# Performance work log

Hardware: AMD Instinct MI355X
Metric: run time of the kernel (lower is better)

The kernel has to match this reference:

```python
import jax, jax.numpy as jnp
import numpy as np
from jax import lax

IMG_W, IMG_H = 800.0, 320.0
NPTS = 72
N_STRIPS = NPTS - 1
MAX_LANES = 4
NUM_PRIORS = 192
STAGES = 3
B = 512
LIOU_LEN = 15.0
CLS_W, XYT_W, IOU_W, SEG_W = 2.0, 0.2, 2.0, 1.0


def smooth_l1(x):
    ax = jnp.abs(x)
    return jnp.where(ax < 1.0, 0.5 * x * x, ax - 0.5)


def pairwise_line_iou(pred_xs, tgt_xs):
    # pred_xs [P,N] pixel xs, tgt_xs [L,N]; returns [P,L]
    px1, px2 = pred_xs - LIOU_LEN, pred_xs + LIOU_LEN
    tx1, tx2 = tgt_xs - LIOU_LEN, tgt_xs + LIOU_LEN
    ovr = jnp.minimum(px2[:, None, :], tx2[None]) - jnp.maximum(px1[:, None, :], tx1[None])
    union = jnp.maximum(px2[:, None, :], tx2[None]) - jnp.minimum(px1[:, None, :], tx1[None])
    invalid = (tgt_xs < 0) | (tgt_xs >= IMG_W)
    ovr = jnp.where(invalid[None], 0.0, ovr)
    union = jnp.where(invalid[None], 0.0, union)
    return ovr.sum(-1) / (union.sum(-1) + 1e-9)


def focal_sum(logits, target):
    # kornia-style softmax focal loss (alpha=0.25, gamma=2), summed
    p = jax.nn.softmax(logits, axis=1) + 1e-8
    focal = -0.25 * (1.0 - p) ** 2 * jnp.log(p)
    oh = jax.nn.one_hot(target, 2, dtype=logits.dtype)
    return (oh * focal).sum()


def per_sample(pred, tgt):
    # pred [P, 6+N], tgt [L, 6+N]
    L = tgt.shape[0]
    f32 = pred.dtype
    valid = tgt[:, 1] == 1.0
    num_t = valid.sum()
    has_t = num_t > 0

    t_xs = tgt[:, 6:]                          # [L,N] pixel xs (-1e5 = invalid)
    pred_xs_px = pred[:, 6:] * (IMG_W - 1.0)   # [P,N]
    iou_pair = pairwise_line_iou(pred_xs_px, t_xs)  # [P,L] (grad flows for loss)

    # ---------- assignment (stop-grad, mirrors CLRNet dynamic_assign) ----------
    pd = lax.stop_gradient(pred)
    pd_xs = pd[:, 6:] * (IMG_W - 1.0)
    inv_t = (t_xs < 0) | (t_xs >= IMG_W)
    t_len = (~inv_t).sum(1).astype(f32)
    dist = jnp.where(inv_t[None], 0.0, jnp.abs(t_xs[None] - pd_xs[:, None, :])).sum(-1)
    dist = dist / (t_len[None] + 1e-9)         # [P,L]

    def norm_score(x):
        m = jnp.max(jnp.where(valid[None], x, -jnp.inf))
        m = jnp.where(has_t, m, 1.0)
        return 1.0 - x / m + 1e-2

    dist_score = norm_score(dist)
    p_xy = jnp.stack([pd[:, 2] * (IMG_H - 1.0), pd[:, 3] * (IMG_W - 1.0)], 1)
    t_xy = jnp.stack([tgt[:, 2] * (IMG_H - 1.0), tgt[:, 3]], 1)
    sd = jnp.sqrt(((p_xy[:, None] - t_xy[None]) ** 2).sum(-1))
    s_score = norm_score(sd)
    th = jnp.abs(pd[:, 4, None] - tgt[None, :, 4]) * 180.0
    th_score = norm_score(th)
    sp = jax.nn.sigmoid(pd[:, :2])
    neg = -jnp.log(1.0 - sp + 1e-12) * 0.75 * sp ** 2
    pos = -jnp.log(sp + 1e-12) * 0.25 * (1.0 - sp) ** 2
    cls_cost = pos[:, 1] - neg[:, 1]           # all gt labels are 1
    cost = -(dist_score * s_score * th_score) ** 2 * 3.0 + cls_cost[:, None]
    cost = jnp.where(valid[None], cost, jnp.inf)

    # dynamic-k (SimOTA-style)
    iou_sg = jnp.where(valid[None], jnp.maximum(lax.stop_gradient(iou_pair), 0.0), 0.0)
    topk = lax.top_k(iou_sg.T, 4)[0]           # [L,4]
    dyn_k = jnp.maximum(topk.sum(1).astype(jnp.int32), 1)
    ranks = jnp.argsort(jnp.argsort(cost, axis=0), axis=0)
    M = (ranks < dyn_k[None]) & valid[None]
    multi = M.sum(1) > 1
    argmin_col = jnp.argmin(cost, axis=1)
    Mf = M.astype(f32)
    Mf = Mf.at[:, 0].set(jnp.where(multi, 0.0, Mf[:, 0]))
    oh_min = jax.nn.one_hot(argmin_col, L, dtype=f32)
    Mf = jnp.where(multi[:, None] & (oh_min > 0), 1.0, Mf)
    n_match = Mf.sum()

    # ---------- cls loss ----------
    cls_target = (Mf.sum(1) > 0).astype(jnp.int32)
    cls_term = focal_sum(pred[:, :2], cls_target) / jnp.where(has_t, num_t.astype(f32), 1.0)

    # ---------- reg yxtl (smooth L1) ----------
    scale = jnp.array([N_STRIPS, IMG_W - 1.0, 180.0, N_STRIPS], dtype=f32)
    pred_yxtl = pred[:, 2:6] * scale           # [P,4]
    tgt3 = jnp.stack([tgt[:, 2] * N_STRIPS, tgt[:, 3], tgt[:, 4] * 180.0], 1)  # [L,3]
    pred_starts = jnp.clip(jnp.round(lax.stop_gradient(pred[:, 2]) * N_STRIPS), 0, N_STRIPS)
    tgt_starts = jnp.round(tgt[:, 2] * N_STRIPS)
    tgt_len_pair = tgt[None, :, 5] - (pred_starts[:, None] - tgt_starts[None, :])  # [P,L]
    sl = smooth_l1(pred_yxtl[:, None, :3] - tgt3[None]).sum(-1) \
       + smooth_l1(pred_yxtl[:, 3][:, None] - tgt_len_pair)
    reg_term = (Mf * sl).sum() / jnp.maximum(n_match * 4.0, 1.0)
    iou_term = (Mf * (1.0 - iou_pair)).sum() / jnp.maximum(n_match, 1.0)
    zero = jnp.zeros((), f32)
    reg_term = jnp.where(has_t, reg_term, zero)
    iou_term = jnp.where(has_t, iou_term, zero)
    return cls_term, reg_term, iou_term


def setup_inputs() -> dict:
    key = jax.random.key(0)
    ks = jax.random.split(key, 8)
    D = 6 + NPTS
    cls = jax.random.normal(ks[0], (STAGES, B, NUM_PRIORS, 2), jnp.float32)
    rest = jax.random.uniform(ks[1], (STAGES, B, NUM_PRIORS, D - 2), dtype=jnp.float32)
    predictions = jnp.concatenate([cls, rest], -1)

    valid = jax.random.uniform(ks[2], (B, MAX_LANES)) < 0.8
    start = jax.random.randint(ks[3], (B, MAX_LANES), 0, 40)
    length = jax.random.randint(ks[4], (B, MAX_LANES), 10, NPTS)
    end = jnp.minimum(start + length, NPTS)
    idx = jnp.arange(NPTS)
    inside = (idx[None, None] >= start[..., None]) & (idx[None, None] < end[..., None]) & valid[..., None]
    xs = jax.random.uniform(ks[5], (B, MAX_LANES, NPTS), minval=0.0, maxval=IMG_W - 1.0)
    xs = jnp.where(inside, xs, -1e5)
    start_x = jnp.take_along_axis(xs, start[..., None], axis=-1)[..., 0]
    theta = jax.random.uniform(ks[6], (B, MAX_LANES), minval=0.3, maxval=0.9)
    vf = valid.astype(jnp.float32)
    neg = jnp.full((B, MAX_LANES), -1e5, jnp.float32)
    targets = jnp.full((B, MAX_LANES, D), -1e5, jnp.float32)
    targets = targets.at[..., 0].set(1.0 - vf)
    targets = targets.at[..., 1].set(vf)
    targets = targets.at[..., 2].set(jnp.where(valid, start.astype(jnp.float32) / N_STRIPS, neg))
    targets = targets.at[..., 3].set(jnp.where(valid, start_x, neg))
    targets = targets.at[..., 4].set(jnp.where(valid, theta, neg))
    targets = targets.at[..., 5].set(jnp.where(valid, (end - start).astype(jnp.float32), neg))
    targets = targets.at[..., 6:].set(xs)

    seg_loss = jax.random.uniform(ks[7], (), dtype=jnp.float32)
    return {"predictions": predictions, "targets": targets, "seg_loss": seg_loss}


def reference(predictions, targets, seg_loss):
    per_batch = jax.vmap(per_sample)
    cls_l = jnp.zeros((), predictions.dtype)
    reg_l = jnp.zeros((), predictions.dtype)
    iou_l = jnp.zeros((), predictions.dtype)
    for s in range(predictions.shape[0]):  # 3 refine stages (fixed)
        c, r, i = per_batch(predictions[s], targets)
        cls_l = cls_l + c.sum()
        reg_l = reg_l + r.sum()
        iou_l = iou_l + i.sum()
    denom = targets.shape[0] * predictions.shape[0]
    cls_l = cls_l / denom
    reg_l = reg_l / denom
    iou_l = iou_l / denom
    return cls_l * CLS_W + reg_l * XYT_W + iou_l * IOU_W + seg_loss * SEG_W
```

## Files before the change

kernel.cpp:

```cpp
#include <hip/hip_runtime.h>
#include <math.h>

constexpr int kNpts   = 72;
constexpr int kPriors = 192;
constexpr int kLanes  = 4;
constexpr int kBatch  = 512;
constexpr int kStages = 3;
constexpr int kD      = 6 + kNpts;
constexpr int kChunkRows = 64;
constexpr int kChunkF = kChunkRows * kD;
constexpr int kChunkV4 = kChunkF / 4;

typedef unsigned long long u64;

__device__ __forceinline__ float smoothL1(float x) {
  float ax = fabsf(x);
  return ax < 1.0f ? 0.5f * x * x : ax - 0.5f;
}

__device__ __forceinline__ unsigned ordF(float f) {
  unsigned b = __float_as_uint(f);
  return (b & 0x80000000u) ? ~b : (b | 0x80000000u);
}

__device__ __forceinline__ void cswapA(u64& a, u64& b) {
  if (b < a) { u64 t = a; a = b; b = t; }
}
__device__ __forceinline__ void cswapD(float& a, float& b) {
  if (b > a) { float t = a; a = b; b = t; }
}
__device__ __forceinline__ u64 umin64(u64 a, u64 b) { return a < b ? a : b; }
__device__ __forceinline__ u64 umax64(u64 a, u64 b) { return a < b ? b : a; }

__global__ void clr_init(const float* __restrict__ seg, float* __restrict__ out) {
  out[0] = seg[0];
}

__global__ __launch_bounds__(192) void clr_loss_kernel(
    const float* __restrict__ pred,
    const float* __restrict__ tgt,
    float* __restrict__ out) {
  const int blk  = blockIdx.x;
  const int b    = blk & (kBatch - 1);
  const int tid  = threadIdx.x;
  const int wav  = tid >> 6;
  const int lane = tid & 63;

  __shared__ alignas(16) float s_buf[2][kChunkF];
  __shared__ float s_tx[kNpts][kLanes];
  __shared__ float s_m [kNpts][kLanes];
  __shared__ float s_hdr[kLanes][6];
  __shared__ float s_cost[kLanes][kPriors];
  __shared__ float s_iou[kLanes][kPriors];
  __shared__ u64   s_k3[kLanes][3];
  __shared__ int   s_dk[kLanes];
  __shared__ float s_sc[3][4];

  const float*  gsrc = pred + (size_t)blk * (kPriors * kD);
  const float4* g4   = (const float4*)gsrc;

  const float* tg = tgt + (size_t)b * kLanes * kD;
  for (int t = tid; t < kLanes * kNpts; t += 192) {
    int j = t / kNpts, k = t - j * kNpts;
    float v = tg[j * kD + 6 + k];
    s_tx[k][j] = v;
    s_m [k][j] = (v >= 0.0f && v < 800.0f) ? 1.0f : 0.0f;
  }
  if (tid < kLanes * 6) {
    int j = tid / 6, c = tid - j * 6;
    s_hdr[j][c] = tg[j * kD + c];
  }
  if (tid < kLanes) {
    s_dk[tid] = 1; s_k3[tid][0] = 0; s_k3[tid][1] = 0; s_k3[tid][2] = 0;
  }

  {
    float4* d4 = (float4*)&s_buf[0][0];
#pragma unroll
    for (int it = 0; it < 6; ++it) d4[it * 192 + tid] = g4[it * 192 + tid];
    if (tid < kChunkV4 - 6 * 192) d4[1152 + tid] = g4[1152 + tid];
  }
  __syncthreads();

  bool validL[kLanes];
  int num_t = 0;
#pragma unroll
  for (int j = 0; j < kLanes; ++j) {
    validL[j] = (s_hdr[j][1] == 1.0f);
    num_t += validL[j] ? 1 : 0;
  }
  const bool has_t = num_t > 0;

  float p0 = 0, p1 = 0, p2v = 0, p3v = 0, p4v = 0, p5v = 0;
  float ds0 = 0, ds1 = 0, ds2 = 0, ds3 = 0;
  for (int p = 0; p < 3; ++p) {
    if (p < 2) {
      float4* d4 = (float4*)&s_buf[(p + 1) & 1][0];
      const float4* s4 = g4 + (p + 1) * kChunkV4;
#pragma unroll
      for (int it = 0; it < 6; ++it) d4[it * 192 + tid] = s4[it * 192 + tid];
      if (tid < kChunkV4 - 6 * 192) d4[1152 + tid] = s4[1152 + tid];
    }
    if (wav == p) {
      const float2* L2 = (const float2*)(&s_buf[p & 1][0] + lane * kD);
      float2 h0 = L2[0], h1 = L2[1], h2 = L2[2];
      p0 = h0.x; p1 = h0.y; p2v = h1.x; p3v = h1.y; p4v = h2.x; p5v = h2.y;
      const float4* tx4 = (const float4*)&s_tx[0][0];
      const float4* m4  = (const float4*)&s_m[0][0];
#pragma unroll
      for (int i = 0; i < 36; ++i) {
        float2 a = L2[3 + i];
        float pA = a.x * 799.0f, pB = a.y * 799.0f;
        float4 tA = tx4[2 * i],     mA = m4[2 * i];
        float4 tB = tx4[2 * i + 1], mB = m4[2 * i + 1];
        ds0 = fmaf(mA.x, fabsf(tA.x - pA), ds0);
        ds1 = fmaf(mA.y, fabsf(tA.y - pA), ds1);
        ds2 = fmaf(mA.z, fabsf(tA.z - pA), ds2);
        ds3 = fmaf(mA.w, fabsf(tA.w - pA), ds3);
        ds0 = fmaf(mB.x, fabsf(tB.x - pB), ds0);
        ds1 = fmaf(mB.y, fabsf(tB.y - pB), ds1);
        ds2 = fmaf(mB.z, fabsf(tB.z - pB), ds2);
        ds3 = fmaf(mB.w, fabsf(tB.w - pB), ds3);
      }
    }
    __syncthreads();
  }
  float dsA[kLanes] = {ds0, ds1, ds2, ds3};

  float iou[kLanes], dist[kLanes], sd[kLanes], th[kLanes];
  float md = -INFINITY, ms = -INFINITY, mt = -INFINITY;
  const float py = p2v * 319.0f, pxc = p3v * 799.0f;
#pragma unroll
  for (int j = 0; j < kLanes; ++j) {
    float tlen = validL[j] ? s_hdr[j][5] : 0.0f;
    float ovr = fmaf(tlen, 30.0f, -dsA[j]);
    float uni = fmaf(tlen, 30.0f,  dsA[j]) + 1e-9f;
    iou[j]  = ovr / uni;
    dist[j] = dsA[j] / (tlen + 1e-9f);
    float dy = py - s_hdr[j][2] * 319.0f;
    float dx = pxc - s_hdr[j][3];
    sd[j] = sqrtf(dy * dy + dx * dx);
    th[j] = fabsf(p4v - s_hdr[j][4]) * 180.0f;
    if (validL[j]) {
      md = fmaxf(md, dist[j]);
      ms = fmaxf(ms, sd[j]);
      mt = fmaxf(mt, th[j]);
    }
  }

#pragma unroll
  for (int off = 32; off; off >>= 1) {
    md = fmaxf(md, __shfl_down(md, off, 64));
    ms = fmaxf(ms, __shfl_down(ms, off, 64));
    mt = fmaxf(mt, __shfl_down(mt, off, 64));
  }
  if (lane == 0) { s_sc[wav][0] = md; s_sc[wav][1] = ms; s_sc[wav][2] = mt; }
  __syncthreads();
  md = fmaxf(fmaxf(s_sc[0][0], s_sc[1][0]), s_sc[2][0]);
  ms = fmaxf(fmaxf(s_sc[0][1], s_sc[1][1]), s_sc[2][1]);
  mt = fmaxf(fmaxf(s_sc[0][2], s_sc[1][2]), s_sc[2][2]);
  if (!has_t) { md = 1.0f; ms = 1.0f; mt = 1.0f; }

  const float sp1  = 1.0f / (1.0f + expf(-p1));
  const float neg1 = -logf(1.0f - sp1 + 1e-12f) * 0.75f * sp1 * sp1;
  const float om1  = 1.0f - sp1;
  const float pos1 = -logf(sp1 + 1e-12f) * 0.25f * om1 * om1;
  const float cls_cost = pos1 - neg1;

  float costr[kLanes];
#pragma unroll
  for (int j = 0; j < kLanes; ++j) {
    s_iou[j][tid] = validL[j] ? fmaxf(iou[j], 0.0f) : 0.0f;
    float c;
    if (validL[j]) {
      float a = (1.0f - dist[j] / md) + 0.01f;
      float s = (1.0f - sd[j] / ms) + 0.01f;
      float t = (1.0f - th[j] / mt) + 0.01f;
      float g = a * s * t;
      c = cls_cost - g * g * 3.0f;
    } else {
      c = INFINITY;
    }
    costr[j] = c;
    s_cost[j][tid] = c;
  }
  __syncthreads();

  for (int t = wav; t < 8; t += 3) {
    const int j = t & 3;
    if (!validL[j]) continue;
    if (t < 4) {
      float c0 = s_cost[j][lane], c1 = s_cost[j][lane + 64], c2 = s_cost[j][lane + 128];
      u64 k0 = ((u64)ordF(c0) << 32) | (unsigned)lane;
      u64 k1 = ((u64)ordF(c1) << 32) | (unsigned)(lane + 64);
      u64 k2 = ((u64)ordF(c2) << 32) | (unsigned)(lane + 128);
      cswapA(k0, k1); cswapA(k0, k2); cswapA(k1, k2);
#pragma unroll
      for (int off = 1; off < 64; off <<= 1) {
        u64 b0 = __shfl_xor(k0, off), b1 = __shfl_xor(k1, off), b2 = __shfl_xor(k2, off);
        u64 x0 = umin64(k0, b0), y0 = umax64(k0, b0);
        u64 x1 = umin64(k1, b1);
        u64 mc = umin64(k2, b2);
        k0 = x0;
        k2 = umin64(umax64(y0, x1), mc);
        k1 = umin64(y0, x1);
      }
      if (lane == 0) { s_k3[j][0] = k0; s_k3[j][1] = k1; s_k3[j][2] = k2; }
    } else {
      float t0 = s_iou[j][lane], t1 = s_iou[j][lane + 64], t2 = s_iou[j][lane + 128];
      float t3 = -1.0f;
      cswapD(t0, t1); cswapD(t0, t2); cswapD(t1, t2);
#pragma unroll
      for (int off = 1; off < 64; off <<= 1) {
        float b0 = __shfl_xor(t0, off), b1 = __shfl_xor(t1, off);
        float b2 = __shfl_xor(t2, off), b3 = __shfl_xor(t3, off);
        float m0 = fmaxf(t0, b3), m1 = fmaxf(t1, b2);
        float m2 = fmaxf(t2, b1), m3 = fmaxf(t3, b0);
        cswapD(m0, m2); cswapD(m1, m3); cswapD(m0, m1); cswapD(m2, m3);
        t0 = m0; t1 = m1; t2 = m2; t3 = m3;
      }
      if (lane == 0) {
        float s = ((t0 + t1) + t2) + t3;
        int dk = (int)s;
        if (dk < 1) dk = 1;
        if (dk > 3) dk = 3;
        s_dk[j] = dk;
      }
    }
  }
  __syncthreads();

  int Mi[kLanes];
  int msum = 0;
#pragma unroll
  for (int j = 0; j < kLanes; ++j) {
    u64 myk = ((u64)ordF(costr[j]) << 32) | (unsigned)tid;
    Mi[j] = (validL[j] && myk <= s_k3[j][s_dk[j] - 1]) ? 1 : 0;
    msum += Mi[j];
  }

  float amin = costr[0];
  int aidx = 0;
#pragma unroll
  for (int j = 1; j < kLanes; ++j)
    if (costr[j] < amin) { amin = costr[j]; aidx = j; }

  float Mf[kLanes];
#pragma unroll
  for (int j = 0; j < kLanes; ++j) Mf[j] = (float)Mi[j];
  if (msum > 1) {
    Mf[0] = 0.0f;
    Mf[aidx] = 1.0f;
  }

  const float mfsum = Mf[0] + Mf[1] + Mf[2] + Mf[3];
  const int cls_t = (mfsum > 0.0f) ? 1 : 0;

  const float mx = fmaxf(p0, p1);
  const float e0 = expf(p0 - mx), e1 = expf(p1 - mx);
  const float inv = 1.0f / (e0 + e1);
  const float q = (cls_t ? e1 : e0) * inv + 1e-8f;
  const float omq = 1.0f - q;
  const float focal = -0.25f * omq * omq * logf(q);

  const float pred_start = fminf(fmaxf(rintf(p2v * 71.0f), 0.0f), 71.0f);
  const float py0 = p2v * 71.0f, py1 = p3v * 799.0f, py2t = p4v * 180.0f, py3 = p5v * 71.0f;
  float regc = 0.0f, iouc = 0.0f;
#pragma unroll
  for (int j = 0; j < kLanes; ++j) {
    if (Mf[j] > 0.0f) {
      float t30 = s_hdr[j][2] * 71.0f;
      float t31 = s_hdr[j][3];
      float t32 = s_hdr[j][4] * 180.0f;
      float tstart = rintf(s_hdr[j][2] * 71.0f);
      float tlp = s_hdr[j][5] - (pred_start - tstart);
      regc += smoothL1(py0 - t30) + smoothL1(py1 - t31) + smoothL1(py2t - t32)
            + smoothL1(py3 - tlp);
      iouc += 1.0f - iou[j];
    }
  }

  float v0 = mfsum, v1 = focal, v2 = regc, v3 = iouc;
#pragma unroll
  for (int off = 32; off; off >>= 1) {
    v0 += __shfl_down(v0, off, 64);
    v1 += __shfl_down(v1, off, 64);
    v2 += __shfl_down(v2, off, 64);
    v3 += __shfl_down(v3, off, 64);
  }
  __syncthreads();
  if (lane == 0) {
    s_sc[wav][0] = v0; s_sc[wav][1] = v1; s_sc[wav][2] = v2; s_sc[wav][3] = v3;
  }
  __syncthreads();

  if (tid == 0) {
    float nm      = s_sc[0][0] + s_sc[1][0] + s_sc[2][0];
    float cls_sum = s_sc[0][1] + s_sc[1][1] + s_sc[2][1];
    float reg_sum = s_sc[0][2] + s_sc[1][2] + s_sc[2][2];
    float iou_sum = s_sc[0][3] + s_sc[1][3] + s_sc[2][3];

    float cls_term = cls_sum / (has_t ? (float)num_t : 1.0f);
    float reg_term = has_t ? reg_sum / fmaxf(nm * 4.0f, 1.0f) : 0.0f;
    float iou_term = has_t ? iou_sum / fmaxf(nm, 1.0f) : 0.0f;

    float sample = 2.0f * cls_term + 0.2f * reg_term + 2.0f * iou_term;
    atomicAdd(out, sample * (1.0f / (float)(kBatch * kStages)));
  }
}

extern "C" void kernel_launch(void* const* d_in, const int* in_sizes, int n_in,
                              void* d_out, int out_size, void* d_ws, size_t ws_size,
                              hipStream_t stream) {
  const float* pred = (const float*)d_in[0];
  const float* tgt  = (const float*)d_in[1];
  const float* seg  = (const float*)d_in[2];
  float* out = (float*)d_out;

  clr_init<<<1, 1, 0, stream>>>(seg, out);
  clr_loss_kernel<<<kStages * kBatch, 192, 0, stream>>>(pred, tgt, out);
}
```

Before: 165.5 us.

## Split each prior row across two threads and load rows directly into registers

```diff
diff --git a/kernel.cpp b/kernel.cpp
--- a/kernel.cpp
+++ b/kernel.cpp
@@ -7,9 +7,6 @@
 constexpr int kBatch  = 512;
 constexpr int kStages = 3;
 constexpr int kD      = 6 + kNpts;
-constexpr int kChunkRows = 64;
-constexpr int kChunkF = kChunkRows * kD;
-constexpr int kChunkV4 = kChunkF / 4;
 
 typedef unsigned long long u64;
 
@@ -36,7 +33,7 @@
   out[0] = seg[0];
 }
 
-__global__ __launch_bounds__(192) void clr_loss_kernel(
+__global__ __launch_bounds__(384) void clr_loss_kernel(
     const float* __restrict__ pred,
     const float* __restrict__ tgt,
     float* __restrict__ out) {
@@ -45,40 +42,44 @@
   const int tid  = threadIdx.x;
   const int wav  = tid >> 6;
   const int lane = tid & 63;
-
-  __shared__ alignas(16) float s_buf[2][kChunkF];
-  __shared__ float s_tx[kNpts][kLanes];
-  __shared__ float s_m [kNpts][kLanes];
-  __shared__ float s_hdr[kLanes][6];
-  __shared__ float s_cost[kLanes][kPriors];
-  __shared__ float s_iou[kLanes][kPriors];
-  __shared__ u64   s_k3[kLanes][3];
-  __shared__ int   s_dk[kLanes];
-  __shared__ float s_sc[3][4];
-
-  const float*  gsrc = pred + (size_t)blk * (kPriors * kD);
-  const float4* g4   = (const float4*)gsrc;
+  const bool prim = (wav < 3);
+  const int  pid  = prim ? tid : tid - 192;
+
+  __shared__ float  s_tx[kNpts][kLanes];
+  __shared__ float  s_m [kNpts][kLanes];
+  __shared__ float  s_hdr[kLanes][6];
+  __shared__ float4 s_part[kPriors];
+  __shared__ float  s_cost[kLanes][kPriors];
+  __shared__ float  s_iou[kLanes][kPriors];
+  __shared__ u64    s_k3[kLanes][3];
+  __shared__ int    s_dk[kLanes];
+  __shared__ float  s_sc[3][4];
 
   const float* tg = tgt + (size_t)b * kLanes * kD;
-  for (int t = tid; t < kLanes * kNpts; t += 192) {
-    int j = t / kNpts, k = t - j * kNpts;
+  if (tid < kLanes * kNpts) {
+    int j = tid / kNpts, k = tid - j * kNpts;
     float v = tg[j * kD + 6 + k];
     s_tx[k][j] = v;
     s_m [k][j] = (v >= 0.0f && v < 800.0f) ? 1.0f : 0.0f;
   }
-  if (tid < kLanes * 6) {
-    int j = tid / 6, c = tid - j * 6;
+  if (tid >= 384 - kLanes * 6) {
+    int t = tid - (384 - kLanes * 6);
+    int j = t / 6, c = t - j * 6;
     s_hdr[j][c] = tg[j * kD + c];
   }
-  if (tid < kLanes) {
-    s_dk[tid] = 1; s_k3[tid][0] = 0; s_k3[tid][1] = 0; s_k3[tid][2] = 0;
-  }
-
-  {
-    float4* d4 = (float4*)&s_buf[0][0];
-#pragma unroll
-    for (int it = 0; it < 6; ++it) d4[it * 192 + tid] = g4[it * 192 + tid];
-    if (tid < kChunkV4 - 6 * 192) d4[1152 + tid] = g4[1152 + tid];
+  if (tid >= 288 && tid < 288 + kLanes) {
+    int j = tid - 288;
+    s_dk[j] = 1; s_k3[j][0] = 0; s_k3[j][1] = 0; s_k3[j][2] = 0;
+  }
+
+  const float2* rowv = (const float2*)(pred + ((size_t)blk * kPriors + pid) * kD);
+  float2 r[20];
+  if (prim) {
+#pragma unroll
+    for (int i = 0; i < 20; ++i) r[i] = rowv[i];
+  } else {
+#pragma unroll
+    for (int i = 0; i < 19; ++i) r[i] = rowv[20 + i];
   }
   __syncthreads();
 
@@ -91,102 +92,111 @@
   }
   const bool has_t = num_t > 0;
 
+  float ds0 = 0, ds1 = 0, ds2 = 0, ds3 = 0;
   float p0 = 0, p1 = 0, p2v = 0, p3v = 0, p4v = 0, p5v = 0;
-  float ds0 = 0, ds1 = 0, ds2 = 0, ds3 = 0;
-  for (int p = 0; p < 3; ++p) {
-    if (p < 2) {
-      float4* d4 = (float4*)&s_buf[(p + 1) & 1][0];
-      const float4* s4 = g4 + (p + 1) * kChunkV4;
-#pragma unroll
-      for (int it = 0; it < 6; ++it) d4[it * 192 + tid] = s4[it * 192 + tid];
-      if (tid < kChunkV4 - 6 * 192) d4[1152 + tid] = s4[1152 + tid];
-    }
-    if (wav == p) {
-      const float2* L2 = (const float2*)(&s_buf[p & 1][0] + lane * kD);
-      float2 h0 = L2[0], h1 = L2[1], h2 = L2[2];
-      p0 = h0.x; p1 = h0.y; p2v = h1.x; p3v = h1.y; p4v = h2.x; p5v = h2.y;
-      const float4* tx4 = (const float4*)&s_tx[0][0];
-      const float4* m4  = (const float4*)&s_m[0][0];
-#pragma unroll
-      for (int i = 0; i < 36; ++i) {
-        float2 a = L2[3 + i];
-        float pA = a.x * 799.0f, pB = a.y * 799.0f;
-        float4 tA = tx4[2 * i],     mA = m4[2 * i];
-        float4 tB = tx4[2 * i + 1], mB = m4[2 * i + 1];
-        ds0 = fmaf(mA.x, fabsf(tA.x - pA), ds0);
-        ds1 = fmaf(mA.y, fabsf(tA.y - pA), ds1);
-        ds2 = fmaf(mA.z, fabsf(tA.z - pA), ds2);
-        ds3 = fmaf(mA.w, fabsf(tA.w - pA), ds3);
-        ds0 = fmaf(mB.x, fabsf(tB.x - pB), ds0);
-        ds1 = fmaf(mB.y, fabsf(tB.y - pB), ds1);
-        ds2 = fmaf(mB.z, fabsf(tB.z - pB), ds2);
-        ds3 = fmaf(mB.w, fabsf(tB.w - pB), ds3);
-      }
-    }
-    __syncthreads();
-  }
-  float dsA[kLanes] = {ds0, ds1, ds2, ds3};
-
-  float iou[kLanes], dist[kLanes], sd[kLanes], th[kLanes];
+  const float4* tx4 = (const float4*)&s_tx[0][0];
+  const float4* m4  = (const float4*)&s_m[0][0];
+  if (prim) {
+    p0 = r[0].x; p1 = r[0].y; p2v = r[1].x; p3v = r[1].y; p4v = r[2].x; p5v = r[2].y;
+#pragma unroll
+    for (int i = 0; i < 17; ++i) {
+      float pA = r[3 + i].x * 799.0f, pB = r[3 + i].y * 799.0f;
+      float4 tA = tx4[2 * i],     mA = m4[2 * i];
+      float4 tB = tx4[2 * i + 1], mB = m4[2 * i + 1];
+      ds0 = fmaf(mA.x, fabsf(tA.x - pA), ds0);
+      ds1 = fmaf(mA.y, fabsf(tA.y - pA), ds1);
+      ds2 = fmaf(mA.z, fabsf(tA.z - pA), ds2);
+      ds3 = fmaf(mA.w, fabsf(tA.w - pA), ds3);
+      ds0 = fmaf(mB.x, fabsf(tB.x - pB), ds0);
+      ds1 = fmaf(mB.y, fabsf(tB.y - pB), ds1);
+      ds2 = fmaf(mB.z, fabsf(tB.z - pB), ds2);
+      ds3 = fmaf(mB.w, fabsf(tB.w - pB), ds3);
+    }
+  } else {
+#pragma unroll
+    for (int i = 0; i < 19; ++i) {
+      float pA = r[i].x * 799.0f, pB = r[i].y * 799.0f;
+      int k = 34 + 2 * i;
+      float4 tA = tx4[k],     mA = m4[k];
+      float4 tB = tx4[k + 1], mB = m4[k + 1];
+      ds0 = fmaf(mA.x, fabsf(tA.x - pA), ds0);
+      ds1 = fmaf(mA.y, fabsf(tA.y - pA), ds1);
+      ds2 = fmaf(mA.z, fabsf(tA.z - pA), ds2);
+      ds3 = fmaf(mA.w, fabsf(tA.w - pA), ds3);
+      ds0 = fmaf(mB.x, fabsf(tB.x - pB), ds0);
+      ds1 = fmaf(mB.y, fabsf(tB.y - pB), ds1);
+      ds2 = fmaf(mB.z, fabsf(tB.z - pB), ds2);
+      ds3 = fmaf(mB.w, fabsf(tB.w - pB), ds3);
+    }
+    s_part[pid] = make_float4(ds0, ds1, ds2, ds3);
+  }
+  __syncthreads();
+
+  float iou[kLanes], dist[kLanes], sd[kLanes], th[kLanes], costr[kLanes];
   float md = -INFINITY, ms = -INFINITY, mt = -INFINITY;
-  const float py = p2v * 319.0f, pxc = p3v * 799.0f;
-#pragma unroll
-  for (int j = 0; j < kLanes; ++j) {
-    float tlen = validL[j] ? s_hdr[j][5] : 0.0f;
-    float ovr = fmaf(tlen, 30.0f, -dsA[j]);
-    float uni = fmaf(tlen, 30.0f,  dsA[j]) + 1e-9f;
-    iou[j]  = ovr / uni;
-    dist[j] = dsA[j] / (tlen + 1e-9f);
-    float dy = py - s_hdr[j][2] * 319.0f;
-    float dx = pxc - s_hdr[j][3];
-    sd[j] = sqrtf(dy * dy + dx * dx);
-    th[j] = fabsf(p4v - s_hdr[j][4]) * 180.0f;
-    if (validL[j]) {
-      md = fmaxf(md, dist[j]);
-      ms = fmaxf(ms, sd[j]);
-      mt = fmaxf(mt, th[j]);
-    }
-  }
-
-#pragma unroll
-  for (int off = 32; off; off >>= 1) {
-    md = fmaxf(md, __shfl_down(md, off, 64));
-    ms = fmaxf(ms, __shfl_down(ms, off, 64));
-    mt = fmaxf(mt, __shfl_down(mt, off, 64));
-  }
-  if (lane == 0) { s_sc[wav][0] = md; s_sc[wav][1] = ms; s_sc[wav][2] = mt; }
-  __syncthreads();
-  md = fmaxf(fmaxf(s_sc[0][0], s_sc[1][0]), s_sc[2][0]);
-  ms = fmaxf(fmaxf(s_sc[0][1], s_sc[1][1]), s_sc[2][1]);
-  mt = fmaxf(fmaxf(s_sc[0][2], s_sc[1][2]), s_sc[2][2]);
-  if (!has_t) { md = 1.0f; ms = 1.0f; mt = 1.0f; }
-
-  const float sp1  = 1.0f / (1.0f + expf(-p1));
-  const float neg1 = -logf(1.0f - sp1 + 1e-12f) * 0.75f * sp1 * sp1;
-  const float om1  = 1.0f - sp1;
-  const float pos1 = -logf(sp1 + 1e-12f) * 0.25f * om1 * om1;
-  const float cls_cost = pos1 - neg1;
-
-  float costr[kLanes];
-#pragma unroll
-  for (int j = 0; j < kLanes; ++j) {
-    s_iou[j][tid] = validL[j] ? fmaxf(iou[j], 0.0f) : 0.0f;
-    float c;
-    if (validL[j]) {
-      float a = (1.0f - dist[j] / md) + 0.01f;
-      float s = (1.0f - sd[j] / ms) + 0.01f;
-      float t = (1.0f - th[j] / mt) + 0.01f;
-      float g = a * s * t;
-      c = cls_cost - g * g * 3.0f;
-    } else {
-      c = INFINITY;
-    }
-    costr[j] = c;
-    s_cost[j][tid] = c;
-  }
-  __syncthreads();
-
-  for (int t = wav; t < 8; t += 3) {
+  if (prim) {
+    float4 q = s_part[pid];
+    float dsA[kLanes] = {ds0 + q.x, ds1 + q.y, ds2 + q.z, ds3 + q.w};
+    const float py = p2v * 319.0f, pxc = p3v * 799.0f;
+#pragma unroll
+    for (int j = 0; j < kLanes; ++j) {
+      float tlen = validL[j] ? s_hdr[j][5] : 0.0f;
+      float ovr = fmaf(tlen, 30.0f, -dsA[j]);
+      float uni = fmaf(tlen, 30.0f,  dsA[j]) + 1e-9f;
+      iou[j]  = ovr / uni;
+      dist[j] = dsA[j] / (tlen + 1e-9f);
+      float dy = py - s_hdr[j][2] * 319.0f;
+      float dx = pxc - s_hdr[j][3];
+      sd[j] = sqrtf(dy * dy + dx * dx);
+      th[j] = fabsf(p4v - s_hdr[j][4]) * 180.0f;
+      if (validL[j]) {
+        md = fmaxf(md, dist[j]);
+        ms = fmaxf(ms, sd[j]);
+        mt = fmaxf(mt, th[j]);
+      }
+    }
+#pragma unroll
+    for (int off = 32; off; off >>= 1) {
+      md = fmaxf(md, __shfl_down(md, off, 64));
+      ms = fmaxf(ms, __shfl_down(ms, off, 64));
+      mt = fmaxf(mt, __shfl_down(mt, off, 64));
+    }
+    if (lane == 0) { s_sc[wav][0] = md; s_sc[wav][1] = ms; s_sc[wav][2] = mt; }
+  }
+  __syncthreads();
+
+  if (prim) {
+    md = fmaxf(fmaxf(s_sc[0][0], s_sc[1][0]), s_sc[2][0]);
+    ms = fmaxf(fmaxf(s_sc[0][1], s_sc[1][1]), s_sc[2][1]);
+    mt = fmaxf(fmaxf(s_sc[0][2], s_sc[1][2]), s_sc[2][2]);
+    if (!has_t) { md = 1.0f; ms = 1.0f; mt = 1.0f; }
+
+    const float sp1  = 1.0f / (1.0f + expf(-p1));
+    const float neg1 = -logf(1.0f - sp1 + 1e-12f) * 0.75f * sp1 * sp1;
+    const float om1  = 1.0f - sp1;
+    const float pos1 = -logf(sp1 + 1e-12f) * 0.25f * om1 * om1;
+    const float cls_cost = pos1 - neg1;
+
+#pragma unroll
+    for (int j = 0; j < kLanes; ++j) {
+      s_iou[j][pid] = validL[j] ? fmaxf(iou[j], 0.0f) : 0.0f;
+      float c;
+      if (validL[j]) {
+        float a = (1.0f - dist[j] / md) + 0.01f;
+        float s = (1.0f - sd[j] / ms) + 0.01f;
+        float t = (1.0f - th[j] / mt) + 0.01f;
+        float g = a * s * t;
+        c = cls_cost - g * g * 3.0f;
+      } else {
+        c = INFINITY;
+      }
+      costr[j] = c;
+      s_cost[j][pid] = c;
+    }
+  }
+  __syncthreads();
+
+  for (int t = wav; t < 8; t += 6) {
     const int j = t & 3;
     if (!validL[j]) continue;
     if (t < 4) {
@@ -230,67 +240,69 @@
   }
   __syncthreads();
 
-  int Mi[kLanes];
-  int msum = 0;
-#pragma unroll
-  for (int j = 0; j < kLanes; ++j) {
-    u64 myk = ((u64)ordF(costr[j]) << 32) | (unsigned)tid;
-    Mi[j] = (validL[j] && myk <= s_k3[j][s_dk[j] - 1]) ? 1 : 0;
-    msum += Mi[j];
-  }
-
-  float amin = costr[0];
-  int aidx = 0;
-#pragma unroll
-  for (int j = 1; j < kLanes; ++j)
-    if (costr[j] < amin) { amin = costr[j]; aidx = j; }
-
-  float Mf[kLanes];
-#pragma unroll
-  for (int j = 0; j < kLanes; ++j) Mf[j] = (float)Mi[j];
-  if (msum > 1) {
-    Mf[0] = 0.0f;
-    Mf[aidx] = 1.0f;
-  }
-
-  const float mfsum = Mf[0] + Mf[1] + Mf[2] + Mf[3];
-  const int cls_t = (mfsum > 0.0f) ? 1 : 0;
-
-  const float mx = fmaxf(p0, p1);
-  const float e0 = expf(p0 - mx), e1 = expf(p1 - mx);
-  const float inv = 1.0f / (e0 + e1);
-  const float q = (cls_t ? e1 : e0) * inv + 1e-8f;
-  const float omq = 1.0f - q;
-  const float focal = -0.25f * omq * omq * logf(q);
-
-  const float pred_start = fminf(fmaxf(rintf(p2v * 71.0f), 0.0f), 71.0f);
-  const float py0 = p2v * 71.0f, py1 = p3v * 799.0f, py2t = p4v * 180.0f, py3 = p5v * 71.0f;
-  float regc = 0.0f, iouc = 0.0f;
-#pragma unroll
-  for (int j = 0; j < kLanes; ++j) {
-    if (Mf[j] > 0.0f) {
-      float t30 = s_hdr[j][2] * 71.0f;
-      float t31 = s_hdr[j][3];
-      float t32 = s_hdr[j][4] * 180.0f;
-      float tstart = rintf(s_hdr[j][2] * 71.0f);
-      float tlp = s_hdr[j][5] - (pred_start - tstart);
-      regc += smoothL1(py0 - t30) + smoothL1(py1 - t31) + smoothL1(py2t - t32)
-            + smoothL1(py3 - tlp);
-      iouc += 1.0f - iou[j];
-    }
-  }
-
-  float v0 = mfsum, v1 = focal, v2 = regc, v3 = iouc;
-#pragma unroll
-  for (int off = 32; off; off >>= 1) {
-    v0 += __shfl_down(v0, off, 64);
-    v1 += __shfl_down(v1, off, 64);
-    v2 += __shfl_down(v2, off, 64);
-    v3 += __shfl_down(v3, off, 64);
-  }
-  __syncthreads();
-  if (lane == 0) {
-    s_sc[wav][0] = v0; s_sc[wav][1] = v1; s_sc[wav][2] = v2; s_sc[wav][3] = v3;
+  float v0 = 0, v1 = 0, v2 = 0, v3 = 0;
+  if (prim) {
+    int Mi[kLanes];
+    int msum = 0;
+#pragma unroll
+    for (int j = 0; j < kLanes; ++j) {
+      u64 myk = ((u64)ordF(costr[j]) << 32) | (unsigned)pid;
+      Mi[j] = (validL[j] && myk <= s_k3[j][s_dk[j] - 1]) ? 1 : 0;
+      msum += Mi[j];
+    }
+
+    float amin = costr[0];
+    int aidx = 0;
+#pragma unroll
+    for (int j = 1; j < kLanes; ++j)
+      if (costr[j] < amin) { amin = costr[j]; aidx = j; }
+
+    float Mf[kLanes];
+#pragma unroll
+    for (int j = 0; j < kLanes; ++j) Mf[j] = (float)Mi[j];
+    if (msum > 1) {
+      Mf[0] = 0.0f;
+      Mf[aidx] = 1.0f;
+    }
+
+    const float mfsum = Mf[0] + Mf[1] + Mf[2] + Mf[3];
+    const int cls_t = (mfsum > 0.0f) ? 1 : 0;
+
+    const float mx = fmaxf(p0, p1);
+    const float e0 = expf(p0 - mx), e1 = expf(p1 - mx);
+    const float inv = 1.0f / (e0 + e1);
+    const float q = (cls_t ? e1 : e0) * inv + 1e-8f;
+    const float omq = 1.0f - q;
+    const float focal = -0.25f * omq * omq * logf(q);
+
+    const float pred_start = fminf(fmaxf(rintf(p2v * 71.0f), 0.0f), 71.0f);
+    const float py0 = p2v * 71.0f, py1 = p3v * 799.0f, py2t = p4v * 180.0f, py3 = p5v * 71.0f;
+    float regc = 0.0f, iouc = 0.0f;
+#pragma unroll
+    for (int j = 0; j < kLanes; ++j) {
+      if (Mf[j] > 0.0f) {
+        float t30 = s_hdr[j][2] * 71.0f;
+        float t31 = s_hdr[j][3];
+        float t32 = s_hdr[j][4] * 180.0f;
+        float tstart = rintf(s_hdr[j][2] * 71.0f);
+        float tlp = s_hdr[j][5] - (pred_start - tstart);
+        regc += smoothL1(py0 - t30) + smoothL1(py1 - t31) + smoothL1(py2t - t32)
+              + smoothL1(py3 - tlp);
+        iouc += 1.0f - iou[j];
+      }
+    }
+
+    v0 = mfsum; v1 = focal; v2 = regc; v3 = iouc;
+#pragma unroll
+    for (int off = 32; off; off >>= 1) {
+      v0 += __shfl_down(v0, off, 64);
+      v1 += __shfl_down(v1, off, 64);
+      v2 += __shfl_down(v2, off, 64);
+      v3 += __shfl_down(v3, off, 64);
+    }
+    if (lane == 0) {
+      s_sc[wav][0] = v0; s_sc[wav][1] = v1; s_sc[wav][2] = v2; s_sc[wav][3] = v3;
+    }
   }
   __syncthreads();
 
@@ -318,5 +330,5 @@
   float* out = (float*)d_out;
 
   clr_init<<<1, 1, 0, stream>>>(seg, out);
-  clr_loss_kernel<<<kStages * kBatch, 192, 0, stream>>>(pred, tgt, out);
-}
+  clr_loss_kernel<<<kStages * kBatch, 384, 0, stream>>>(pred, tgt, out);
+}
```

New measurement: 163.4 us. About the same (-1.3%).
